# Optimization experiments

Measured on AMD Instinct MI355X. Metric: run time of the kernel, lower is better.

Reference implementation:

```python
import jax, jax.numpy as jnp
import numpy as np

N = 50000          # total points
C = 256            # channels
H = 8              # heads
D = C // H         # head dim = 32
W = 256            # window size
STRIDE = 128
LENGTHS = [12500, 12500, 12500, 12500]
HID = 512          # ffn hidden = 2.0 * C
EPS = 1e-5


def _build_windows():
    """numpy port of build_windows_1d: returns (M, W) indices and bool mask."""
    idxs, masks = [], []
    start = 0
    for L in LENGTHS:
        n_windows = (L - 1) // STRIDE + 1
        for i in range(n_windows):
            s = i * STRIDE
            b = min(L, s + W)
            cur_len = b - s
            loc = np.arange(s, b, dtype=np.int32) + start
            if W - cur_len > 0:
                loc = np.concatenate([loc, np.full(W - cur_len, loc[-1], dtype=np.int32)])
            m = np.zeros(W, dtype=bool)
            m[:cur_len] = True
            idxs.append(loc)
            masks.append(m)
        start += L
    return np.stack(idxs, 0), np.stack(masks, 0)


def setup_inputs() -> dict:
    key = jax.random.key(0)
    ks = jax.random.split(key, 8)
    def p(k, shape):
        return jax.random.normal(k, shape, dtype=jnp.float32) * 0.02
    win_idx_np, win_mask_np = _build_windows()
    return {
        "x": jax.random.normal(ks[0], (N, C), dtype=jnp.float32),
        "win_idx": jnp.asarray(win_idx_np, dtype=jnp.int32),
        "win_mask": jnp.asarray(win_mask_np),
        "norm1_g": jnp.ones((C,), jnp.float32), "norm1_b": jnp.zeros((C,), jnp.float32),
        "qkv_w": p(ks[1], (C, 3 * C)),
        "proj_w": p(ks[2], (C, C)), "proj_b": jnp.zeros((C,), jnp.float32),
        "ca_norm_g": jnp.ones((C,), jnp.float32), "ca_norm_b": jnp.zeros((C,), jnp.float32),
        "ca_qkv_w": p(ks[3], (C, 3 * C)), "ca_qkv_b": jnp.zeros((3 * C,), jnp.float32),
        "ca_proj_w": p(ks[4], (C, C)), "ca_proj_b": jnp.zeros((C,), jnp.float32),
        "norm2_g": jnp.ones((C,), jnp.float32), "norm2_b": jnp.zeros((C,), jnp.float32),
        "ffn_w1": p(ks[5], (C, HID)), "ffn_b1": jnp.zeros((HID,), jnp.float32),
        "ffn_ln_g": jnp.ones((HID,), jnp.float32), "ffn_ln_b": jnp.zeros((HID,), jnp.float32),
        "ffn_w2": p(ks[6], (HID, C)), "ffn_b2": jnp.zeros((C,), jnp.float32),
    }


def _ln(x, g, b):
    m = jnp.mean(x, axis=-1, keepdims=True)
    v = jnp.mean((x - m) ** 2, axis=-1, keepdims=True)
    return (x - m) * jax.lax.rsqrt(v + EPS) * g + b


def reference(x, win_idx, win_mask,
              norm1_g, norm1_b, qkv_w, proj_w, proj_b,
              ca_norm_g, ca_norm_b, ca_qkv_w, ca_qkv_b, ca_proj_w, ca_proj_b,
              norm2_g, norm2_b, ffn_w1, ffn_b1, ffn_ln_g, ffn_ln_b, ffn_w2, ffn_b2):
    M, Wn = win_idx.shape
    scale = D ** -0.5
    maskf = win_mask[..., None].astype(x.dtype)          # [M, W, 1]

    x_in = _ln(x, norm1_g, norm1_b)                      # [N, C]
    xw = x_in[win_idx]                                   # gather windows [M, W, C]

    # --- Stream A: per-window SDPA ---
    qkv = xw @ qkv_w                                     # [M, W, 3C]
    q, k, v = [t.reshape(M, Wn, H, D).transpose(0, 2, 1, 3)
               for t in jnp.split(qkv, 3, axis=-1)]      # each [M, H, W, D]
    scores = jnp.einsum('mhqd,mhkd->mhqk', q, k) * scale
    scores = jnp.where(win_mask[:, None, None, :], scores, -jnp.inf)
    attn = jax.nn.softmax(scores, axis=-1)
    out = jnp.einsum('mhqk,mhkd->mhqd', attn, v).transpose(0, 2, 1, 3).reshape(M, Wn, C)
    out = (out @ proj_w + proj_b) * maskf                # masked per-window output

    # --- Stream B: centroid attention over M window centroids ---
    wc = jnp.maximum(win_mask.sum(-1, keepdims=True).astype(x.dtype), 1.0)  # [M, 1]
    cent = (xw * maskf).sum(1) / wc                      # [M, C]
    cx = _ln(cent, ca_norm_g, ca_norm_b)
    cqkv = cx @ ca_qkv_w + ca_qkv_b
    cq, ck, cv = [t.reshape(M, H, D).transpose(1, 0, 2)
                  for t in jnp.split(cqkv, 3, axis=-1)]  # each [H, M, D]
    cs = jnp.einsum('hqd,hkd->hqk', cq, ck) * scale
    co = jnp.einsum('hqk,hkd->hqd', jax.nn.softmax(cs, -1), cv)
    co = co.transpose(1, 0, 2).reshape(M, C)
    cent_out = cent + co @ ca_proj_w + ca_proj_b         # residual + proj

    gctx = cent_out[:, None, :] * maskf                  # broadcast global ctx [M, W, C]

    # --- scatter-add back with overlap averaging ---
    total = (out + gctx).reshape(-1, C)
    flat_idx = win_idx.reshape(-1)
    y = jnp.zeros_like(x).at[flat_idx].add(total)
    counts = jnp.zeros((x.shape[0], 1), x.dtype).at[flat_idx].add(
        win_mask.reshape(-1, 1).astype(x.dtype))
    x_out = x + y / jnp.maximum(counts, 1.0)

    # --- FFN (LayerNorm variant) ---
    h1 = _ln(x_out, norm2_g, norm2_b) @ ffn_w1 + ffn_b1
    h1 = jax.nn.relu(_ln(h1, ffn_ln_g, ffn_ln_b))
    return x_out + h1 @ ffn_w2 + ffn_b2
```

## Files before the change

### kernel.cpp

```cpp
#include <hip/hip_runtime.h>

typedef unsigned short ushort;
typedef unsigned int uint;
typedef __attribute__((ext_vector_type(4))) float f32x4;
typedef __attribute__((ext_vector_type(16))) float f32x16;
typedef __attribute__((ext_vector_type(8))) short bf16x8;
typedef __attribute__((ext_vector_type(4))) uint uint32x4;
typedef __attribute__((ext_vector_type(2))) uint uint2v;

#define NPTS 50000
#define C 256
#define CH3 768
#define H 8
#define D 32
#define WW 256
#define HID 512
#define EPSV 1e-5f
#define QK_SCALE 0.17677669529663687f
#define LOG2E 1.4426950408889634f
#define SC_LOG2 (QK_SCALE * LOG2E)

#define BM 128
#define BN 128
#define BK 64
#define NGEMM_QKV 2346
#define NCENT 392
#define NATT 3136

__device__ inline float bf2f(ushort u) { uint i = ((uint)u) << 16; float f; __builtin_memcpy(&f, &i, 4); return f; }
__device__ inline float bflo(uint u) { uint i = u << 16; float f; __builtin_memcpy(&f, &i, 4); return f; }
__device__ inline float bfhi(uint u) { uint i = u & 0xffff0000u; float f; __builtin_memcpy(&f, &i, 4); return f; }
__device__ inline ushort f2bf(float f) {
  uint i; __builtin_memcpy(&i, &f, 4);
  uint r = i + 0x7fffu + ((i >> 16) & 1u);
  return (ushort)(r >> 16);
}
__device__ inline uint pk2bf(float a, float b) { return (uint)f2bf(a) | ((uint)f2bf(b) << 16); }

__device__ __forceinline__ void gload16(const ushort* g, const ushort* l) {
  __builtin_amdgcn_global_load_lds(
      (const __attribute__((address_space(1))) unsigned int*)(unsigned long long)g,
      (__attribute__((address_space(3))) unsigned int*)(unsigned int)(unsigned long long)l,
      16, 0, 0);
}

__device__ __forceinline__ int xcd_swz(int orig, int nwg) {
  int q8 = nwg >> 3, r8 = nwg & 7;
  int xcd = orig & 7, sub = orig >> 3;
  return (xcd < r8 ? xcd * (q8 + 1) : r8 * (q8 + 1) + (xcd - r8) * q8) + sub;
}

#define BLOCK_REDUCE_2(sv, s2v)                                            \
  {                                                                        \
    _Pragma("unroll")                                                      \
    for (int o_ = 1; o_ < 64; o_ <<= 1) {                                  \
      sv  += __shfl_xor(sv, o_);                                           \
      s2v += __shfl_xor(s2v, o_);                                          \
    }                                                                      \
    __shared__ float ls_[4], ls2_[4];                                      \
    int wid_ = threadIdx.x >> 6;                                           \
    if ((threadIdx.x & 63) == 0) { ls_[wid_] = sv; ls2_[wid_] = s2v; }     \
    __syncthreads();                                                       \
    sv  = ls_[0] + ls_[1] + ls_[2] + ls_[3];                               \
    s2v = ls2_[0] + ls2_[1] + ls2_[2] + ls2_[3];                           \
  }

template <int EPI>
__device__ __forceinline__ void gemm_body(ushort* SMEM, int bid,
                                          const ushort* __restrict__ A,
                                          const ushort* __restrict__ Bt,
                                          void* __restrict__ outp,
                                          const float* __restrict__ bias,
                                          int Mrows, int Ncols, int K) {
  ushort* As = SMEM;
  ushort* Bs = SMEM + BM * BK;
  int t = threadIdx.x;
  int nbn = Ncols >> 7;
  int bm = bid / nbn, bn = bid - bm * nbn;
  int l = t & 63, wv = t >> 6;
  int wr = wv >> 1, wcid = wv & 1;
  int l15 = l & 15, l4 = l >> 4;
  int lr = l >> 3;
  int csrc = ((l & 7) ^ lr) << 3;
  f32x4 acc[4][4];
#pragma unroll
  for (int i = 0; i < 4; ++i)
#pragma unroll
    for (int j = 0; j < 4; ++j) acc[i][j] = (f32x4){0.f, 0.f, 0.f, 0.f};

  int nks = K >> 6;
  for (int ks = 0; ks < nks; ++ks) {
    if (ks) __syncthreads();
#pragma unroll
    for (int i = 0; i < 4; ++i) {
      int rloc = wv * 8 + lr + i * 32;
      int growA = min(bm * BM + rloc, Mrows - 1);
      gload16(&A[(size_t)growA * K + (ks << 6) + csrc], &As[(wv * 8 + i * 32) * BK]);
      gload16(&Bt[(size_t)(bn * BN + rloc) * K + (ks << 6) + csrc], &Bs[(wv * 8 + i * 32) * BK]);
    }
    __syncthreads();
#pragma unroll
    for (int kk = 0; kk < 2; ++kk) {
      bf16x8 af[4], bfr[4];
#pragma unroll
      for (int i = 0; i < 4; ++i) {
        int ra = wr * 64 + i * 16 + l15;
        int ca = (l4 + kk * 4) ^ (ra & 7);
        af[i] = *(const bf16x8*)&As[ra * BK + (ca << 3)];
        int rb = wcid * 64 + i * 16 + l15;
        int cb = (l4 + kk * 4) ^ (rb & 7);
        bfr[i] = *(const bf16x8*)&Bs[rb * BK + (cb << 3)];
      }
      __builtin_amdgcn_s_setprio(1);
#pragma unroll
      for (int i = 0; i < 4; ++i)
#pragma unroll
        for (int j = 0; j < 4; ++j)
          acc[i][j] = __builtin_amdgcn_mfma_f32_16x16x32_bf16(af[i], bfr[j], acc[i][j], 0, 0, 0);
      __builtin_amdgcn_s_setprio(0);
    }
  }

  const int CS = 136;
  ushort* Cs = SMEM;
#pragma unroll
  for (int pass = 0; pass < 2; ++pass) {
    __syncthreads();
    if (wr == pass) {
#pragma unroll
      for (int i = 0; i < 4; ++i)
#pragma unroll
        for (int j = 0; j < 4; ++j)
#pragma unroll
          for (int r = 0; r < 4; ++r) {
            int rl = i * 16 + l4 * 4 + r;
            int cl = wcid * 64 + j * 16 + l15;
            float v = acc[i][j][r];
            if (EPI >= 1) v += bias[bn * BN + cl];
            Cs[rl * CS + cl] = f2bf(v);
          }
    }
    __syncthreads();
    int rl = t >> 2;
    int cq = (t & 3) * 32;
    int grow = bm * BM + pass * 64 + rl;
    if (grow < Mrows) {
      if (EPI <= 1) {
        ushort* orow = (ushort*)outp + (size_t)grow * Ncols + bn * BN + cq;
#pragma unroll
        for (int s = 0; s < 4; ++s)
          *(uint4*)(orow + s * 8) = *(const uint4*)&Cs[rl * CS + cq + s * 8];
      } else {
        float* orow = (float*)outp + (size_t)grow * Ncols + bn * BN + cq;
#pragma unroll
        for (int s = 0; s < 8; ++s) {
          float4 ov = *(float4*)(orow + s * 4);
          const ushort* cp = &Cs[rl * CS + cq + s * 4];
          ov.x += bf2f(cp[0]); ov.y += bf2f(cp[1]);
          ov.z += bf2f(cp[2]); ov.w += bf2f(cp[3]);
          *(float4*)(orow + s * 4) = ov;
        }
      }
    }
  }
}

template <int EPI>
__global__ __launch_bounds__(256, 4) void gemm_bf16(
    const ushort* __restrict__ A, const ushort* __restrict__ Bt, void* __restrict__ outp,
    const float* __restrict__ bias, int Mrows, int Ncols, int K) {
  __shared__ ushort SMEM[(BM + BN) * BK];
  int bid = xcd_swz(blockIdx.x, gridDim.x);
  gemm_body<EPI>(SMEM, bid, A, Bt, outp, bias, Mrows, Ncols, K);
}

__global__ __launch_bounds__(256) void pre_kernel(
    const float* __restrict__ qkv_w, const float* __restrict__ proj_w,
    const float* __restrict__ w1, const float* __restrict__ w2,
    ushort* __restrict__ qkv_wt, ushort* __restrict__ proj_wt,
    ushort* __restrict__ w1t, ushort* __restrict__ w2t,
    const float* __restrict__ x, const float* __restrict__ g, const float* __restrict__ b,
    ushort* __restrict__ xout) {
  int bid = blockIdx.x;
  if (bid < 128) {
    __shared__ float tile[64][65];
    const float* w; ushort* wt; int K, N, boff; float scale; int n_hi;
    if (bid < 48)      { w = qkv_w;  wt = qkv_wt;  K = C;   N = CH3; boff = 0;  scale = SC_LOG2; n_hi = C; }
    else if (bid < 64) { w = proj_w; wt = proj_wt; K = C;   N = C;   boff = 48; scale = 1.f; n_hi = 0; }
    else if (bid < 96) { w = w1;     wt = w1t;     K = C;   N = HID; boff = 64; scale = 1.f; n_hi = 0; }
    else               { w = w2;     wt = w2t;     K = HID; N = C;   boff = 96; scale = 1.f; n_hi = 0; }
    int lb = bid - boff;
    int nbn = N >> 6;
    int bk = lb / nbn, bn = lb - bk * nbn;
    int c = threadIdx.x & 63, r4 = threadIdx.x >> 6;
#pragma unroll
    for (int rr = 0; rr < 16; ++rr) {
      int r = rr * 4 + r4;
      tile[r][c] = w[(size_t)(bk * 64 + r) * N + bn * 64 + c];
    }
    __syncthreads();
#pragma unroll
    for (int rr = 0; rr < 16; ++rr) {
      int r = rr * 4 + r4;
      int n = bn * 64 + r;
      float s = (n < n_hi) ? scale : 1.f;
      wt[(size_t)n * K + bk * 64 + c] = f2bf(tile[c][r] * s);
    }
  } else {
    int wv = threadIdx.x >> 6, lane = threadIdx.x & 63;
    int row = (bid - 128) * 4 + wv;
    float4 v = ((const float4*)(x + (size_t)row * C))[lane];
    float s = v.x + v.y + v.z + v.w;
    float s2 = v.x * v.x + v.y * v.y + v.z * v.z + v.w * v.w;
#pragma unroll
    for (int o = 1; o < 64; o <<= 1) { s += __shfl_xor(s, o); s2 += __shfl_xor(s2, o); }
    float mean = s * (1.0f / C);
    float var = s2 * (1.0f / C) - mean * mean;
    float rs = rsqrtf(var + EPSV);
    float4 gv = ((const float4*)g)[lane];
    float4 bv = ((const float4*)b)[lane];
    uint2 pk;
    pk.x = pk2bf((v.x - mean) * rs * gv.x + bv.x, (v.y - mean) * rs * gv.y + bv.y);
    pk.y = pk2bf((v.z - mean) * rs * gv.z + bv.z, (v.w - mean) * rs * gv.w + bv.w);
    ((uint2*)(xout + (size_t)row * C))[lane] = pk;
  }
}

__global__ __launch_bounds__(256, 4) void qkv_cent_kernel(
    const ushort* __restrict__ xb, const int* __restrict__ win_idx,
    const float* __restrict__ lng, const float* __restrict__ lnb,
    const float* __restrict__ caw, const float* __restrict__ cab,
    float* __restrict__ cent, float* __restrict__ cqkv, float* __restrict__ kT,
    int* __restrict__ wc_i, const ushort* __restrict__ qkv_wt, ushort* __restrict__ qkvb, int M) {
  __shared__ ushort SMEM[(BM + BN) * BK];
  int bid = blockIdx.x;
  if (bid < NCENT) {
    float* fbase = (float*)SMEM;
    float (*red)[257] = (float(*)[257])fbase;
    float* cxl = fbase + 8 * 257;
    int m = bid, t = threadIdx.x;
    int i0 = win_idx[m * WW];
    int iL = win_idx[m * WW + WW - 1];
    int wc = iL - i0 + 1;
    if (t == 0) wc_i[m] = wc;
    int rg = t >> 5, cg = t & 31;
    float acc[8] = {0.f, 0.f, 0.f, 0.f, 0.f, 0.f, 0.f, 0.f};
    for (int r = rg; r < wc; r += 8) {
      uint4 u = *(const uint4*)(xb + (size_t)(i0 + r) * C + cg * 8);
      acc[0] += bflo(u.x); acc[1] += bfhi(u.x);
      acc[2] += bflo(u.y); acc[3] += bfhi(u.y);
      acc[4] += bflo(u.z); acc[5] += bfhi(u.z);
      acc[6] += bflo(u.w); acc[7] += bfhi(u.w);
    }
#pragma unroll
    for (int j = 0; j < 8; ++j) red[rg][cg * 8 + j] = acc[j];
    __syncthreads();
    float sum = red[0][t];
#pragma unroll
    for (int k = 1; k < 8; ++k) sum += red[k][t];
    float cv = sum / (float)wc;
    cent[m * C + t] = cv;
    float s = cv, s2 = cv * cv;
    BLOCK_REDUCE_2(s, s2);
    float mean = s * (1.0f / C);
    float var = s2 * (1.0f / C) - mean * mean;
    float rs = rsqrtf(var + EPSV);
    cxl[t] = (cv - mean) * rs * lng[t] + lnb[t];
    __syncthreads();
    for (int j = t; j < CH3; j += 256) {
      float a = cab[j];
      for (int c2 = 0; c2 < C; ++c2) a += cxl[c2] * caw[(size_t)c2 * CH3 + j];
      cqkv[(size_t)m * CH3 + j] = a;
      if (j >= C && j < 2 * C) kT[(size_t)(j - C) * M + m] = a;
    }
  } else {
    int g = xcd_swz(bid - NCENT, NGEMM_QKV);
    gemm_body<0>(SMEM, g, xb, qkv_wt, qkvb, nullptr, NPTS, CH3, C);
  }
}

__global__ __launch_bounds__(256) void attn_cent_kernel(
    const ushort* __restrict__ qkv, const int* __restrict__ win_idx,
    const int* __restrict__ wc_i, ushort* __restrict__ ao,
    const float* __restrict__ cqkv, const float* __restrict__ kT,
    const float* __restrict__ cent,
    const float* __restrict__ pw, const float* __restrict__ pb,
    float* __restrict__ cent_o, int* __restrict__ slots, int M) {
  __shared__ char SM[37376];
  int bid = blockIdx.x;
  int t = threadIdx.x;

  if (bid < NCENT) {
    float* fbase = (float*)SM;
    float (*p_lds)[400] = (float(*)[400])fbase;
    float* co_lds = fbase + 8 * 400;
    int wv = t >> 6, lane = t & 63;
    int mq = bid;
#pragma unroll
    for (int pp = 0; pp < 2; ++pp) {
      int h = wv * 2 + pp;
      const float* qp = cqkv + (size_t)mq * CH3 + h * D;
      float q[D];
#pragma unroll
      for (int d = 0; d < D; ++d) q[d] = qp[d] * SC_LOG2;
      float s[7];
      float mi = -3.0e38f;
#pragma unroll
      for (int j = 0; j < 7; ++j) {
        int mk = lane + 64 * j;
        s[j] = -3.0e38f;
        if (mk < M) {
          float a = 0.f;
#pragma unroll
          for (int d = 0; d < D; ++d) a += q[d] * kT[(size_t)(h * D + d) * M + mk];
          s[j] = a;
          mi = fmaxf(mi, a);
        }
      }
#pragma unroll
      for (int off = 1; off < 64; off <<= 1) mi = fmaxf(mi, __shfl_xor(mi, off));
      float li = 0.f;
#pragma unroll
      for (int j = 0; j < 7; ++j) {
        int mk = lane + 64 * j;
        if (mk < M) { float pv = exp2f(s[j] - mi); li += pv; p_lds[h][mk] = pv; }
      }
#pragma unroll
      for (int off = 1; off < 64; off <<= 1) li += __shfl_xor(li, off);
      int d = lane & 31, hpp = lane >> 5;
      int half = (M + 1) / 2;
      int k0 = hpp * half, k1 = min(M, k0 + half);
      float o = 0.f;
      for (int k = k0; k < k1; ++k)
        o += p_lds[h][k] * cqkv[(size_t)k * CH3 + 2 * C + h * D + d];
      o += __shfl_xor(o, 32);
      if (lane < 32) co_lds[h * D + d] = o / li;
    }
    __syncthreads();
    float a = pb[t] + cent[(size_t)mq * C + t];
    for (int k = 0; k < C; ++k) a += co_lds[k] * pw[(size_t)k * C + t];
    cent_o[(size_t)mq * C + t] = a;
    return;
  }
  if (bid < 2 * NCENT) {
    int m = bid - NCENT;
    int wc = wc_i[m];
    int i0 = win_idx[m * WW];
    if (t < wc) slots[2 * (i0 + t) + (t >= 128 ? 0 : 1)] = m * WW + t;
    return;
  }

  ushort* K_lds = (ushort*)SM;
  uint* Vt = (uint*)(SM + 20480);
  int abid = xcd_swz(bid - 2 * NCENT, NATT);
  int m = abid >> 3, h = abid & 7;
  int wcv = wc_i[m];
  int i0 = win_idx[m * WW];
  int lane = t & 63, wq = t >> 6;
  int l31 = lane & 31, hp = lane >> 5;

  bf16x8 qf[2][2];
#pragma unroll
  for (int qb = 0; qb < 2; ++qb) {
    int qrow = i0 + min(wq * 64 + qb * 32 + l31, wcv - 1);
#pragma unroll
    for (int c = 0; c < 2; ++c)
      qf[qb][c] = *(const bf16x8*)(qkv + (size_t)qrow * CH3 + h * D + c * 16 + hp * 8);
  }

  if (t >= 128) {
    int base = (t - 128) * 2;
#pragma unroll
    for (int rr = 0; rr < 2; ++rr) {
      int row = base + rr;
      const uint4* src = (const uint4*)(qkv + (size_t)(i0 + min(row, wcv - 1)) * CH3 + C + h * D);
      *(uint4*)&K_lds[row * 40 + 0]  = src[0];
      *(uint4*)&K_lds[row * 40 + 8]  = src[1];
      *(uint4*)&K_lds[row * 40 + 16] = src[2];
      *(uint4*)&K_lds[row * 40 + 24] = src[3];
    }
  } else {
    int k0 = t * 2;
    const uint* s0 = (const uint*)(qkv + (size_t)(i0 + min(k0, wcv - 1)) * CH3 + 2 * C + h * D);
    const uint* s1 = (const uint*)(qkv + (size_t)(i0 + min(k0 + 1, wcv - 1)) * CH3 + 2 * C + h * D);
#pragma unroll
    for (int w2 = 0; w2 < 16; ++w2) {
      uint a = s0[w2], b = s1[w2];
      Vt[(2 * w2) * 132 + t] = (a & 0xffffu) | (b << 16);
      Vt[(2 * w2 + 1) * 132 + t] = (a >> 16) | (b & 0xffff0000u);
    }
  }
  __syncthreads();

  const f32x16 zv = {0.f, 0.f, 0.f, 0.f, 0.f, 0.f, 0.f, 0.f,
                     0.f, 0.f, 0.f, 0.f, 0.f, 0.f, 0.f, 0.f};
  f32x16 O0 = zv, O1 = zv;
  float l0 = 0.f, l1 = 0.f;
  int ntile = (wcv + 31) >> 5;

  for (int kt = 0; kt < ntile; ++kt) {
    int kbase = kt * 32;
    bf16x8 ka0 = *(const bf16x8*)&K_lds[(kbase + l31) * 40 + hp * 8];
    bf16x8 ka1 = *(const bf16x8*)&K_lds[(kbase + l31) * 40 + 16 + hp * 8];
    uint4 v0raw = *(const uint4*)&Vt[l31 * 132 + kt * 16 + hp * 4];
    uint4 v1raw = *(const uint4*)&Vt[l31 * 132 + kt * 16 + 8 + hp * 4];
    bf16x8 vb0 = __builtin_bit_cast(bf16x8, v0raw);
    bf16x8 vb1 = __builtin_bit_cast(bf16x8, v1raw);
    bool partial = (kbase + 32 > wcv);

    auto qbody = [&](const bf16x8& q0, const bf16x8& q1, f32x16& O, float& lq) {
      __builtin_amdgcn_s_setprio(1);
      f32x16 st = __builtin_amdgcn_mfma_f32_32x32x16_bf16(ka0, q0, zv, 0, 0, 0);
      st = __builtin_amdgcn_mfma_f32_32x32x16_bf16(ka1, q1, st, 0, 0, 0);
      __builtin_amdgcn_s_setprio(0);
      if (partial) {
        int kb_h = kbase + 4 * hp;
#pragma unroll
        for (int r = 0; r < 16; ++r) {
          int crow = (r & 3) + 8 * (r >> 2);
          st[r] = (kb_h + crow >= wcv) ? -3.0e38f : st[r];
        }
      }
      float p[16];
      float ls = 0.f;
#pragma unroll
      for (int r = 0; r < 16; ++r) { p[r] = exp2f(st[r]); ls += p[r]; }
      lq += ls;
      uint w[8];
#pragma unroll
      for (int i = 0; i < 8; ++i) {
        uint o;
        asm("v_cvt_pk_bf16_f32 %0, %1, %2" : "=v"(o) : "v"(p[2 * i]), "v"(p[2 * i + 1]));
        w[i] = o;
      }
#if __has_builtin(__builtin_amdgcn_permlane32_swap)
      uint2v s02 = __builtin_amdgcn_permlane32_swap(w[0], w[2], false, false);
      uint2v s13 = __builtin_amdgcn_permlane32_swap(w[1], w[3], false, false);
      uint2v s46 = __builtin_amdgcn_permlane32_swap(w[4], w[6], false, false);
      uint2v s57 = __builtin_amdgcn_permlane32_swap(w[5], w[7], false, false);
      uint32x4 pa0u = {s02.x, s13.x, s02.y, s13.y};
      uint32x4 pa1u = {s46.x, s57.x, s46.y, s57.y};
#else
      uint sw0 = __shfl_xor((int)w[0], 32), sw1 = __shfl_xor((int)w[1], 32);
      uint sw2 = __shfl_xor((int)w[2], 32), sw3 = __shfl_xor((int)w[3], 32);
      uint sw4 = __shfl_xor((int)w[4], 32), sw5 = __shfl_xor((int)w[5], 32);
      uint sw6 = __shfl_xor((int)w[6], 32), sw7 = __shfl_xor((int)w[7], 32);
      uint32x4 pa0u = {hp ? sw2 : w[0], hp ? sw3 : w[1], hp ? w[2] : sw0, hp ? w[3] : sw1};
      uint32x4 pa1u = {hp ? sw6 : w[4], hp ? sw7 : w[5], hp ? w[6] : sw4, hp ? w[7] : sw5};
#endif
      bf16x8 pa0 = __builtin_bit_cast(bf16x8, pa0u);
      bf16x8 pa1 = __builtin_bit_cast(bf16x8, pa1u);
      __builtin_amdgcn_s_setprio(1);
      O = __builtin_amdgcn_mfma_f32_32x32x16_bf16(pa0, vb0, O, 0, 0, 0);
      O = __builtin_amdgcn_mfma_f32_32x32x16_bf16(pa1, vb1, O, 0, 0, 0);
      __builtin_amdgcn_s_setprio(0);
    };
    qbody(qf[0][0], qf[0][1], O0, l0);
    qbody(qf[1][0], qf[1][1], O1, l1);
  }

  auto epi = [&](f32x16& O, float lq, int qb) {
    float lt = lq + __shfl_xor(lq, 32);
    float inv = 1.f / lt;
#pragma unroll
    for (int r = 0; r < 16; ++r) {
      int qi = (r & 3) + 8 * (r >> 2) + 4 * hp;
      float iv = __shfl(inv, qi);
      int row = m * WW + wq * 64 + qb * 32 + qi;
      ao[(size_t)row * C + h * D + l31] = f2bf(O[r] * iv);
    }
  };
  epi(O0, l0, 0);
  epi(O1, l1, 1);
}

__global__ __launch_bounds__(256) void combine_ln_kernel(
    const float* __restrict__ x, const int* __restrict__ slots,
    const ushort* __restrict__ pout, const float* __restrict__ cent_o,
    const float* __restrict__ g, const float* __restrict__ b,
    float* __restrict__ xout, ushort* __restrict__ lnx) {
  int wv = threadIdx.x >> 6, lane = threadIdx.x & 63;
  int i = blockIdx.x * 4 + wv;
  int e0 = slots[2 * i], e1 = slots[2 * i + 1];
  float4 xv = ((const float4*)(x + (size_t)i * C))[lane];
  float a0 = 0.f, a1 = 0.f, a2 = 0.f, a3 = 0.f, cnt = 0.f;
  if (e0 >= 0) {
    uint2 pv = ((const uint2*)(pout + (size_t)e0 * C))[lane];
    float4 cv = ((const float4*)(cent_o + (size_t)(e0 >> 8) * C))[lane];
    a0 += bflo(pv.x) + cv.x; a1 += bfhi(pv.x) + cv.y;
    a2 += bflo(pv.y) + cv.z; a3 += bfhi(pv.y) + cv.w;
    cnt += 1.f;
  }
  if (e1 >= 0) {
    uint2 pv = ((const uint2*)(pout + (size_t)e1 * C))[lane];
    float4 cv = ((const float4*)(cent_o + (size_t)(e1 >> 8) * C))[lane];
    a0 += bflo(pv.x) + cv.x; a1 += bfhi(pv.x) + cv.y;
    a2 += bflo(pv.y) + cv.z; a3 += bfhi(pv.y) + cv.w;
    cnt += 1.f;
  }
  float inv = cnt > 0.f ? 1.f / cnt : 0.f;
  float o0 = xv.x + a0 * inv, o1 = xv.y + a1 * inv;
  float o2 = xv.z + a2 * inv, o3 = xv.w + a3 * inv;
  float s = o0 + o1 + o2 + o3;
  float s2 = o0 * o0 + o1 * o1 + o2 * o2 + o3 * o3;
#pragma unroll
  for (int o = 1; o < 64; o <<= 1) { s += __shfl_xor(s, o); s2 += __shfl_xor(s2, o); }
  float mean = s * (1.0f / C);
  float var = s2 * (1.0f / C) - mean * mean;
  float rs = rsqrtf(var + EPSV);
  ((float4*)(xout + (size_t)i * C))[lane] = make_float4(o0, o1, o2, o3);
  float4 gv = ((const float4*)g)[lane];
  float4 bv = ((const float4*)b)[lane];
  uint2 pk;
  pk.x = pk2bf((o0 - mean) * rs * gv.x + bv.x, (o1 - mean) * rs * gv.y + bv.y);
  pk.y = pk2bf((o2 - mean) * rs * gv.z + bv.z, (o3 - mean) * rs * gv.w + bv.w);
  ((uint2*)(lnx + (size_t)i * C))[lane] = pk;
}

__global__ __launch_bounds__(256) void hln_relu_kernel(ushort* __restrict__ h,
                                                       const float* __restrict__ g,
                                                       const float* __restrict__ b) {
  int wv = threadIdx.x >> 6, lane = threadIdx.x & 63;
  int i = blockIdx.x * 4 + wv;
  uint4 u = ((const uint4*)(h + (size_t)i * HID))[lane];
  float v[8] = {bflo(u.x), bfhi(u.x), bflo(u.y), bfhi(u.y),
                bflo(u.z), bfhi(u.z), bflo(u.w), bfhi(u.w)};
  float s = 0.f, s2 = 0.f;
#pragma unroll
  for (int j = 0; j < 8; ++j) { s += v[j]; s2 += v[j] * v[j]; }
#pragma unroll
  for (int o = 1; o < 64; o <<= 1) { s += __shfl_xor(s, o); s2 += __shfl_xor(s2, o); }
  float mean = s * (1.0f / HID);
  float var = s2 * (1.0f / HID) - mean * mean;
  float rs = rsqrtf(var + EPSV);
  float4 g0 = ((const float4*)g)[lane * 2], g1 = ((const float4*)g)[lane * 2 + 1];
  float4 b0 = ((const float4*)b)[lane * 2], b1 = ((const float4*)b)[lane * 2 + 1];
  float ga[8] = {g0.x, g0.y, g0.z, g0.w, g1.x, g1.y, g1.z, g1.w};
  float ba[8] = {b0.x, b0.y, b0.z, b0.w, b1.x, b1.y, b1.z, b1.w};
  float r[8];
#pragma unroll
  for (int j = 0; j < 8; ++j) r[j] = fmaxf((v[j] - mean) * rs * ga[j] + ba[j], 0.f);
  uint4 outu = make_uint4(pk2bf(r[0], r[1]), pk2bf(r[2], r[3]),
                          pk2bf(r[4], r[5]), pk2bf(r[6], r[7]));
  ((uint4*)(h + (size_t)i * HID))[lane] = outu;
}

extern "C" void kernel_launch(void* const* d_in, const int* in_sizes, int n_in,
                              void* d_out, int out_size, void* d_ws, size_t ws_size,
                              hipStream_t stream) {
  (void)n_in; (void)ws_size; (void)out_size;
  const float* x         = (const float*)d_in[0];
  const int*   win_idx   = (const int*)d_in[1];
  const float* norm1_g   = (const float*)d_in[3];
  const float* norm1_b   = (const float*)d_in[4];
  const float* qkv_w     = (const float*)d_in[5];
  const float* proj_w    = (const float*)d_in[6];
  const float* proj_b    = (const float*)d_in[7];
  const float* ca_norm_g = (const float*)d_in[8];
  const float* ca_norm_b = (const float*)d_in[9];
  const float* ca_qkv_w  = (const float*)d_in[10];
  const float* ca_qkv_b  = (const float*)d_in[11];
  const float* ca_proj_w = (const float*)d_in[12];
  const float* ca_proj_b = (const float*)d_in[13];
  const float* norm2_g   = (const float*)d_in[14];
  const float* norm2_b   = (const float*)d_in[15];
  const float* ffn_w1    = (const float*)d_in[16];
  const float* ffn_b1    = (const float*)d_in[17];
  const float* ffn_ln_g  = (const float*)d_in[18];
  const float* ffn_ln_b  = (const float*)d_in[19];
  const float* ffn_w2    = (const float*)d_in[20];
  const float* ffn_b2    = (const float*)d_in[21];

  const int M = in_sizes[1] / WW;

  char* p = (char*)d_ws;
  auto alloc = [&](size_t bytes) { char* r = p; p += (bytes + 255) & ~(size_t)255; return r; };
  ushort* x_in_b = (ushort*)alloc((size_t)NPTS * C * 2);
  ushort* qkvb   = (ushort*)alloc((size_t)NPTS * CH3 * 2);
  ushort* aob    = (ushort*)alloc((size_t)M * WW * C * 2);
  ushort* pout   = (ushort*)alloc((size_t)M * WW * C * 2);
  int*   slots   = (int*)  alloc((size_t)NPTS * 2 * 4);
  int*   wc_i    = (int*)  alloc((size_t)M * 4);
  float* cent    = (float*)alloc((size_t)M * C * 4);
  float* cqkv    = (float*)alloc((size_t)M * CH3 * 4);
  float* kT      = (float*)alloc((size_t)C * M * 4);
  float* cent_o  = (float*)alloc((size_t)M * C * 4);
  ushort* qkv_wt = (ushort*)alloc((size_t)CH3 * C * 2);
  ushort* proj_wt= (ushort*)alloc((size_t)C * C * 2);
  ushort* w1t    = (ushort*)alloc((size_t)HID * C * 2);
  ushort* w2t    = (ushort*)alloc((size_t)C * HID * 2);
  float* yout    = (float*)d_out;

  hipMemsetAsync(slots, 0xFF, (size_t)NPTS * 2 * 4, stream);

  pre_kernel<<<128 + NPTS / 4, 256, 0, stream>>>(
      qkv_w, proj_w, ffn_w1, ffn_w2, qkv_wt, proj_wt, w1t, w2t,
      x, norm1_g, norm1_b, x_in_b);

  qkv_cent_kernel<<<NCENT + NGEMM_QKV, 256, 0, stream>>>(
      x_in_b, win_idx, ca_norm_g, ca_norm_b, ca_qkv_w, ca_qkv_b,
      cent, cqkv, kT, wc_i, qkv_wt, qkvb, M);

  attn_cent_kernel<<<2 * NCENT + NATT, 256, 0, stream>>>(
      qkvb, win_idx, wc_i, aob, cqkv, kT, cent, ca_proj_w, ca_proj_b, cent_o, slots, M);

  gemm_bf16<1><<<(M * WW / BM) * (C / BN), 256, 0, stream>>>(aob, proj_wt, pout, proj_b,
                                                             M * WW, C, C);
  ushort* lnx = x_in_b;
  combine_ln_kernel<<<NPTS / 4, 256, 0, stream>>>(x, slots, pout, cent_o, norm2_g, norm2_b,
                                                  yout, lnx);
  ushort* h1 = qkvb;
  const int gm = (NPTS + BM - 1) / BM;
  gemm_bf16<1><<<gm * (HID / BN), 256, 0, stream>>>(lnx, w1t, h1, ffn_b1,
                                                    NPTS, HID, C);
  hln_relu_kernel<<<NPTS / 4, 256, 0, stream>>>(h1, ffn_ln_g, ffn_ln_b);
  gemm_bf16<2><<<gm * (C / BN), 256, 0, stream>>>(h1, w2t, yout, ffn_b2,
                                                  NPTS, C, HID);
}
```

Baseline: 402.7 us.

## Move centroid projection into proj GEMM launch, use raw exp2, raise occupancy

The centroid-attention output projection (a serial 256-step dot per thread) moves out of the attention kernel into a new combined kernel. There it runs as extra blocks alongside the window proj GEMM, so it no longer stretches the attention kernel's tail. The attention output now goes through a new global buffer instead of LDS. It also swaps exp2f for the raw hardware exp2 builtin and raises launch_bounds min-blocks from 4 to 5 on the GEMM kernels, which may cap registers and cause spills.

```diff
diff --git a/kernel.cpp b/kernel.cpp
--- a/kernel.cpp
+++ b/kernel.cpp
@@ -26,6 +26,13 @@
 #define NGEMM_QKV 2346
 #define NCENT 392
 #define NATT 3136
+#define NPROJ 1568
+
+#if __has_builtin(__builtin_amdgcn_exp2f)
+#define EXP2R(x) __builtin_amdgcn_exp2f(x)
+#else
+#define EXP2R(x) exp2f(x)
+#endif
 
 __device__ inline float bf2f(ushort u) { uint i = ((uint)u) << 16; float f; __builtin_memcpy(&f, &i, 4); return f; }
 __device__ inline float bflo(uint u) { uint i = u << 16; float f; __builtin_memcpy(&f, &i, 4); return f; }
@@ -166,7 +173,7 @@
 }
 
 template <int EPI>
-__global__ __launch_bounds__(256, 4) void gemm_bf16(
+__global__ __launch_bounds__(256, 5) void gemm_bf16(
     const ushort* __restrict__ A, const ushort* __restrict__ Bt, void* __restrict__ outp,
     const float* __restrict__ bias, int Mrows, int Ncols, int K) {
   __shared__ ushort SMEM[(BM + BN) * BK];
@@ -226,7 +233,7 @@
   }
 }
 
-__global__ __launch_bounds__(256, 4) void qkv_cent_kernel(
+__global__ __launch_bounds__(256, 5) void qkv_cent_kernel(
     const ushort* __restrict__ xb, const int* __restrict__ win_idx,
     const float* __restrict__ lng, const float* __restrict__ lnb,
     const float* __restrict__ caw, const float* __restrict__ cab,
@@ -283,17 +290,13 @@
     const ushort* __restrict__ qkv, const int* __restrict__ win_idx,
     const int* __restrict__ wc_i, ushort* __restrict__ ao,
     const float* __restrict__ cqkv, const float* __restrict__ kT,
-    const float* __restrict__ cent,
-    const float* __restrict__ pw, const float* __restrict__ pb,
-    float* __restrict__ cent_o, int* __restrict__ slots, int M) {
+    float* __restrict__ co, int* __restrict__ slots, int M) {
   __shared__ char SM[37376];
   int bid = blockIdx.x;
   int t = threadIdx.x;
 
   if (bid < NCENT) {
-    float* fbase = (float*)SM;
-    float (*p_lds)[400] = (float(*)[400])fbase;
-    float* co_lds = fbase + 8 * 400;
+    float (*p_lds)[400] = (float(*)[400])(float*)SM;
     int wv = t >> 6, lane = t & 63;
     int mq = bid;
 #pragma unroll
@@ -323,7 +326,7 @@
 #pragma unroll
       for (int j = 0; j < 7; ++j) {
         int mk = lane + 64 * j;
-        if (mk < M) { float pv = exp2f(s[j] - mi); li += pv; p_lds[h][mk] = pv; }
+        if (mk < M) { float pv = EXP2R(s[j] - mi); li += pv; p_lds[h][mk] = pv; }
       }
 #pragma unroll
       for (int off = 1; off < 64; off <<= 1) li += __shfl_xor(li, off);
@@ -334,12 +337,8 @@
       for (int k = k0; k < k1; ++k)
         o += p_lds[h][k] * cqkv[(size_t)k * CH3 + 2 * C + h * D + d];
       o += __shfl_xor(o, 32);
-      if (lane < 32) co_lds[h * D + d] = o / li;
-    }
-    __syncthreads();
-    float a = pb[t] + cent[(size_t)mq * C + t];
-    for (int k = 0; k < C; ++k) a += co_lds[k] * pw[(size_t)k * C + t];
-    cent_o[(size_t)mq * C + t] = a;
+      if (lane < 32) co[(size_t)mq * C + h * D + d] = o / li;
+    }
     return;
   }
   if (bid < 2 * NCENT) {
@@ -424,7 +423,7 @@
       float p[16];
       float ls = 0.f;
 #pragma unroll
-      for (int r = 0; r < 16; ++r) { p[r] = exp2f(st[r]); ls += p[r]; }
+      for (int r = 0; r < 16; ++r) { p[r] = EXP2R(st[r]); ls += p[r]; }
       lq += ls;
       uint w[8];
 #pragma unroll
@@ -474,6 +473,28 @@
   epi(O1, l1, 1);
 }
 
+__global__ __launch_bounds__(256, 5) void proj_cent_kernel(
+    const ushort* __restrict__ aob, const ushort* __restrict__ proj_wt,
+    ushort* __restrict__ pout, const float* __restrict__ proj_b,
+    const float* __restrict__ co, const float* __restrict__ cent,
+    const float* __restrict__ pw, const float* __restrict__ pb,
+    float* __restrict__ cent_o, int M) {
+  __shared__ ushort SMEM[(BM + BN) * BK];
+  int bid = blockIdx.x;
+  if (bid < NCENT) {
+    float* co_lds = (float*)SMEM;
+    int mq = bid, t = threadIdx.x;
+    co_lds[t] = co[(size_t)mq * C + t];
+    __syncthreads();
+    float a = pb[t] + cent[(size_t)mq * C + t];
+    for (int k = 0; k < C; ++k) a += co_lds[k] * pw[(size_t)k * C + t];
+    cent_o[(size_t)mq * C + t] = a;
+    return;
+  }
+  int g = xcd_swz(bid - NCENT, NPROJ);
+  gemm_body<1>(SMEM, g, aob, proj_wt, pout, proj_b, M * WW, C, C);
+}
+
 __global__ __launch_bounds__(256) void combine_ln_kernel(
     const float* __restrict__ x, const int* __restrict__ slots,
     const ushort* __restrict__ pout, const float* __restrict__ cent_o,
@@ -584,6 +605,7 @@
   float* cent    = (float*)alloc((size_t)M * C * 4);
   float* cqkv    = (float*)alloc((size_t)M * CH3 * 4);
   float* kT      = (float*)alloc((size_t)C * M * 4);
+  float* co      = (float*)alloc((size_t)M * C * 4);
   float* cent_o  = (float*)alloc((size_t)M * C * 4);
   ushort* qkv_wt = (ushort*)alloc((size_t)CH3 * C * 2);
   ushort* proj_wt= (ushort*)alloc((size_t)C * C * 2);
@@ -602,10 +624,11 @@
       cent, cqkv, kT, wc_i, qkv_wt, qkvb, M);
 
   attn_cent_kernel<<<2 * NCENT + NATT, 256, 0, stream>>>(
-      qkvb, win_idx, wc_i, aob, cqkv, kT, cent, ca_proj_w, ca_proj_b, cent_o, slots, M);
-
-  gemm_bf16<1><<<(M * WW / BM) * (C / BN), 256, 0, stream>>>(aob, proj_wt, pout, proj_b,
-                                                             M * WW, C, C);
+      qkvb, win_idx, wc_i, aob, cqkv, kT, co, slots, M);
+
+  proj_cent_kernel<<<NCENT + NPROJ, 256, 0, stream>>>(
+      aob, proj_wt, pout, proj_b, co, cent, ca_proj_w, ca_proj_b, cent_o, M);
+
   ushort* lnx = x_in_b;
   combine_ln_kernel<<<NPTS / 4, 256, 0, stream>>>(x, slots, pout, cent_o, norm2_g, norm2_b,
                                                   yout, lnx);
```

Measured after the change: 640.7 us. +59.1%, slower.
